# Optimization experiments

Hardware: AMD Instinct MI355X
Metric: run time of the kernel (lower is better)

Reference implementation:

```python
import jax, jax.numpy as jnp
import numpy as np

B, IH, IW = 16, 32, 32
N = IH * IW
HEADS, DIM_HEAD = 8, 64
INNER = HEADS * DIM_HEAD  # 512
INP, OUP = 512, 512
SCALE = DIM_HEAD ** -0.5


def _relative_index():
    # replicate torch.meshgrid (ij) -> coords [2, N]
    yy, xx = np.meshgrid(np.arange(IH), np.arange(IW), indexing='ij')
    coords = np.stack([yy.reshape(-1), xx.reshape(-1)])  # [2, N]
    rel = coords[:, :, None] - coords[:, None, :]        # [2, N, N]
    rel[0] += IH - 1
    rel[1] += IW - 1
    rel[0] *= 2 * IW - 1
    return jnp.asarray(rel.sum(0).reshape(-1), dtype=jnp.int32)  # [N*N]


def setup_inputs() -> dict:
    key = jax.random.key(0)
    k1, k2, k3, k4, k5 = jax.random.split(key, 5)
    x = jax.random.normal(k1, (B, N, INP), dtype=jnp.float32)
    W_qkv = jax.random.normal(k2, (INP, 3 * INNER), dtype=jnp.float32) * (INP ** -0.5)
    # table is initialized to zeros in the module; use small randn so bias path is exercised
    rel_table = jax.random.normal(k3, ((2 * IH - 1) * (2 * IW - 1), HEADS), dtype=jnp.float32) * 0.02
    W_out = jax.random.normal(k4, (INNER, OUP), dtype=jnp.float32) * (INNER ** -0.5)
    b_out = jax.random.normal(k5, (OUP,), dtype=jnp.float32) * 0.02
    return {
        'x': x,
        'W_qkv': W_qkv,
        'rel_table': rel_table,
        'W_out': W_out,
        'b_out': b_out,
        'rel_index': _relative_index(),
    }


def reference(x, W_qkv, rel_table, W_out, b_out, rel_index):
    b, n, _ = x.shape
    qkv = x @ W_qkv                                            # [b, n, 3*inner]
    q, k, v = jnp.split(qkv, 3, axis=-1)
    def to_heads(t):
        return t.reshape(b, n, HEADS, DIM_HEAD).transpose(0, 2, 1, 3)  # [b, h, n, d]
    q, k, v = to_heads(q), to_heads(k), to_heads(v)
    dots = jnp.einsum('bhnd,bhmd->bhnm', q, k) * SCALE         # [b, h, n, n]
    bias = rel_table[rel_index].reshape(n, n, HEADS).transpose(2, 0, 1)[None]  # [1, h, n, n]
    attn = jax.nn.softmax(dots + bias, axis=-1)
    out = jnp.einsum('bhnm,bhmd->bhnd', attn, v)               # [b, h, n, d]
    out = out.transpose(0, 2, 1, 3).reshape(b, n, INNER)       # [b, n, inner]
    return out @ W_out + b_out
```

## Files before the change

### kernel.cpp

```cpp
#include <hip/hip_runtime.h>
#include <math.h>

#define BATCH 16
#define NTOK 1024
#define HEADS 8
#define DHEAD 64
#define INNER 512
#define QKV_COLS 1536
#define SCALE_L2E 0.1803368801111244f
#define LOG2E 1.4426950408889634f

#if __has_builtin(__builtin_amdgcn_exp2f)
#define EXP2F(x) __builtin_amdgcn_exp2f(x)
#else
#define EXP2F(x) __expf((x) * 0.6931471805599453f)
#endif

typedef _Float16 f16x8 __attribute__((ext_vector_type(8)));
typedef _Float16 f16x4 __attribute__((ext_vector_type(4)));
typedef float f32x4 __attribute__((ext_vector_type(4)));

#define MFMA32(a, b, c) __builtin_amdgcn_mfma_f32_16x16x32_f16(a, b, c, 0, 0, 0)
#define MFMA16(a, b, c) __builtin_amdgcn_mfma_f32_16x16x16f16(a, b, c, 0, 0, 0)

__device__ __forceinline__ void glds16(const void* g, void* l) {
    __builtin_amdgcn_global_load_lds(
        (const __attribute__((address_space(1))) unsigned int*)g,
        (__attribute__((address_space(3))) unsigned int*)l, 16, 0, 0);
}

#define XV (BATCH * NTOK * INNER / 4)
#define WQ (INNER * QKV_COLS)
#define WO (INNER * INNER)

__global__ __launch_bounds__(256)
void convert_inputs(const float* __restrict__ x, const float* __restrict__ Wq,
                    const float* __restrict__ Wo, _Float16* __restrict__ x_h,
                    _Float16* __restrict__ Wq_t, _Float16* __restrict__ Wo_t) {
    int idx = blockIdx.x * 256 + threadIdx.x;
    if (idx < XV) {
        float4 v = ((const float4*)x)[idx];
        f16x4 h;
        h[0] = (_Float16)v.x; h[1] = (_Float16)v.y;
        h[2] = (_Float16)v.z; h[3] = (_Float16)v.w;
        *(f16x4*)(x_h + (size_t)idx * 4) = h;
    } else if (idx < XV + WQ) {
        int i = idx - XV;
        int n = i >> 9, k = i & 511;
        Wq_t[i] = (_Float16)Wq[k * QKV_COLS + n];
    } else if (idx < XV + WQ + WO) {
        int i = idx - XV - WQ;
        int n = i >> 9, k = i & 511;
        Wo_t[i] = (_Float16)Wo[k * INNER + n];
    }
}

template<bool OUT_F16, bool ADD_BIAS>
__global__ __launch_bounds__(256)
void gemm_f16(const _Float16* __restrict__ A, const _Float16* __restrict__ Bt,
              const float* __restrict__ bias, void* __restrict__ Cout,
              int M, int N, int K) {
    __shared__ _Float16 As[128 * 32];
    __shared__ _Float16 Bs[128 * 32];

    const int t    = threadIdx.x;
    const int l    = t & 63;
    const int w    = t >> 6;
    const int wm   = w >> 1;
    const int wn   = w & 1;
    const int quad = l >> 4;
    const int lrow = l & 15;
    const size_t row0 = (size_t)blockIdx.y * 128;
    const size_t col0 = (size_t)blockIdx.x * 128;

    const int srow = t >> 2;
    const int sch  = t & 3;

    f32x4 acc[4][4] = {};

    for (int k0 = 0; k0 < K; k0 += 32) {
        __syncthreads();
        glds16(A + (row0 + srow) * K + k0 + sch * 8,            (char*)As + t * 16);
        glds16(A + (row0 + 64 + srow) * K + k0 + sch * 8,       (char*)As + 4096 + t * 16);
        glds16(Bt + (col0 + srow) * K + k0 + sch * 8,           (char*)Bs + t * 16);
        glds16(Bt + (col0 + 64 + srow) * K + k0 + sch * 8,      (char*)Bs + 4096 + t * 16);
        __syncthreads();

        f16x8 af[4], bf[4];
#pragma unroll
        for (int i = 0; i < 4; ++i)
            af[i] = *(const f16x8*)(As + (wm * 64 + i * 16 + lrow) * 32 + quad * 8);
#pragma unroll
        for (int j = 0; j < 4; ++j)
            bf[j] = *(const f16x8*)(Bs + (wn * 64 + j * 16 + lrow) * 32 + quad * 8);
#pragma unroll
        for (int i = 0; i < 4; ++i)
#pragma unroll
            for (int j = 0; j < 4; ++j)
                acc[i][j] = __builtin_amdgcn_mfma_f32_16x16x32_f16(af[i], bf[j], acc[i][j], 0, 0, 0);
    }

#pragma unroll
    for (int i = 0; i < 4; ++i) {
#pragma unroll
        for (int j = 0; j < 4; ++j) {
            size_t r = row0 + wm * 64 + i * 16 + quad * 4;
            size_t c = col0 + wn * 64 + j * 16 + lrow;
#pragma unroll
            for (int reg = 0; reg < 4; ++reg) {
                float v = acc[i][j][reg];
                if (OUT_F16) {
                    ((_Float16*)Cout)[(r + reg) * N + c] = (_Float16)v;
                } else {
                    if (ADD_BIAS) v += bias[c];
                    ((float*)Cout)[(r + reg) * N + c] = v;
                }
            }
        }
    }
}

__global__ __launch_bounds__(256)
void transpose_v(const _Float16* __restrict__ qkv, _Float16* __restrict__ vt) {
    __shared__ _Float16 T[64][72];
    const int t  = threadIdx.x;
    const int j0 = blockIdx.x * 64;
    const int h  = blockIdx.y, bb = blockIdx.z;
    const int jr = t >> 2;
    const int dc = (t & 3) * 16;
    const _Float16* src = qkv + ((size_t)bb * NTOK + j0 + jr) * QKV_COLS + 2 * INNER + h * DHEAD + dc;
    f16x8 v0 = *(const f16x8*)src;
    f16x8 v1 = *(const f16x8*)(src + 8);
#pragma unroll
    for (int e = 0; e < 8; ++e) { T[jr][dc + e] = v0[e]; T[jr][dc + 8 + e] = v1[e]; }
    __syncthreads();
    const int dr = t >> 2;
    const int jc = (t & 3) * 16;
    f16x8 o0, o1;
#pragma unroll
    for (int e = 0; e < 8; ++e) { o0[e] = T[jc + e][dr]; o1[e] = T[jc + 8 + e][dr]; }
    _Float16* dst = vt + (((size_t)bb * HEADS + h) * 64 + dr) * NTOK + j0 + jc;
    *(f16x8*)dst = o0;
    *(f16x8*)(dst + 8) = o1;
}

__global__ __launch_bounds__(256, 4)
void attn_f16_v5(const _Float16* __restrict__ qkv, const _Float16* __restrict__ vt,
                 const float* __restrict__ rel_table, _Float16* __restrict__ out) {
    __shared__ _Float16 Ks[2][64 * 64];
    __shared__ _Float16 Vs[2][64 * 64];
    __shared__ _Float16 biasH[3969];

    const int t    = threadIdx.x;
    const int l    = t & 63;
    const int w    = t >> 6;
    const int quad = l >> 4;
    const int lrow = l & 15;
    const int h    = blockIdx.y;
    const int bb   = blockIdx.z;
    const int qr0  = blockIdx.x * 128 + w * 32;

    for (int idx = t; idx < 3969; idx += 256)
        biasH[idx] = (_Float16)(rel_table[idx * HEADS + h] * LOG2E);

    const size_t tokbase = (size_t)bb * NTOK;

    f16x8 aq[2][2];
#pragma unroll
    for (int mt = 0; mt < 2; ++mt)
#pragma unroll
        for (int ksi = 0; ksi < 2; ++ksi)
            aq[mt][ksi] = *(const f16x8*)(qkv + (tokbase + qr0 + mt * 16 + lrow) * QKV_COLS
                                          + h * DHEAD + ksi * 32 + quad * 8);

    f32x4 O[2][4] = {};
    float l0 = 0.f, l1 = 0.f;

    const int bconst = ((qr0 >> 5) + 31) * 63 + 31 + lrow - quad * 4;

    const int kr  = t >> 3;
    const int ksl = t & 7;
    const _Float16* kbase = qkv + tokbase * QKV_COLS + INNER + h * DHEAD;
    const _Float16* vbase = vt + ((size_t)(bb * HEADS + h) * 64) * NTOK;

    auto stage = [&](int jt, int bufi) {
        const int j0s = jt * 64;
        const int swz = (ksl ^ (kr & 7)) * 8;
        glds16(kbase + (size_t)(j0s + kr) * QKV_COLS + swz,      (char*)Ks[bufi] + t * 16);
        glds16(kbase + (size_t)(j0s + 32 + kr) * QKV_COLS + swz, (char*)Ks[bufi] + 4096 + t * 16);
        glds16(vbase + (size_t)kr * NTOK + j0s + swz,            (char*)Vs[bufi] + t * 16);
        glds16(vbase + (size_t)(32 + kr) * NTOK + j0s + swz,     (char*)Vs[bufi] + 4096 + t * 16);
    };

    stage(0, 0);

    for (int jt = 0; jt < 16; ++jt) {
        const int buf = jt & 1;
        __syncthreads();
        if (jt < 15) stage(jt + 1, buf ^ 1);

#pragma unroll
        for (int jn = 0; jn < 4; ++jn) {
            const int row = jn * 16 + lrow;
            f32x4 S0 = {}, S1 = {};
#pragma unroll
            for (int ksi = 0; ksi < 2; ++ksi) {
                f16x8 bk = *(const f16x8*)(Ks[buf] + row * 64 + (((ksi * 4 + quad) ^ (row & 7)) * 8));
                S0 = MFMA32(bk, aq[0][ksi], S0);
                S1 = MFMA32(bk, aq[1][ksi], S1);
            }

            const int base0 = bconst - (jt * 2 + (jn >> 1)) * 63 - (jn & 1) * 16;
            f16x4 pb0, pb1;
            {
                float p0 = EXP2F(fmaf(S0[0], SCALE_L2E, (float)biasH[base0 - 0]));
                float p1 = EXP2F(fmaf(S0[1], SCALE_L2E, (float)biasH[base0 - 1]));
                float p2 = EXP2F(fmaf(S0[2], SCALE_L2E, (float)biasH[base0 - 2]));
                float p3 = EXP2F(fmaf(S0[3], SCALE_L2E, (float)biasH[base0 - 3]));
                l0 += (p0 + p1) + (p2 + p3);
                pb0[0] = (_Float16)p0; pb0[1] = (_Float16)p1;
                pb0[2] = (_Float16)p2; pb0[3] = (_Float16)p3;
            }
            {
                const int base1 = base0 + 16;
                float p0 = EXP2F(fmaf(S1[0], SCALE_L2E, (float)biasH[base1 - 0]));
                float p1 = EXP2F(fmaf(S1[1], SCALE_L2E, (float)biasH[base1 - 1]));
                float p2 = EXP2F(fmaf(S1[2], SCALE_L2E, (float)biasH[base1 - 2]));
                float p3 = EXP2F(fmaf(S1[3], SCALE_L2E, (float)biasH[base1 - 3]));
                l1 += (p0 + p1) + (p2 + p3);
                pb1[0] = (_Float16)p0; pb1[1] = (_Float16)p1;
                pb1[2] = (_Float16)p2; pb1[3] = (_Float16)p3;
            }

#pragma unroll
            for (int dn = 0; dn < 4; ++dn) {
                const int d = dn * 16 + lrow;
                f16x4 av = *(const f16x4*)(Vs[buf] + d * 64
                              + (((jn * 2 + (quad >> 1)) ^ (d & 7)) * 8) + (quad & 1) * 4);
                O[0][dn] = MFMA16(av, pb0, O[0][dn]);
                O[1][dn] = MFMA16(av, pb1, O[1][dn]);
            }
        }
    }

#pragma unroll
    for (int mt = 0; mt < 2; ++mt) {
        float s = mt ? l1 : l0;
        s += __shfl_xor(s, 16);
        s += __shfl_xor(s, 32);
        const float inv = 1.f / s;
        const size_t orow = (tokbase + qr0 + mt * 16 + lrow) * INNER + h * DHEAD;
#pragma unroll
        for (int dn = 0; dn < 4; ++dn) {
            const f32x4 o = O[mt][dn];
            f16x4 ov;
            ov[0] = (_Float16)(o[0] * inv); ov[1] = (_Float16)(o[1] * inv);
            ov[2] = (_Float16)(o[2] * inv); ov[3] = (_Float16)(o[3] * inv);
            *(f16x4*)(out + orow + dn * 16 + quad * 4) = ov;
        }
    }
}

extern "C" void kernel_launch(void* const* d_in, const int* in_sizes, int n_in,
                              void* d_out, int out_size, void* d_ws, size_t ws_size,
                              hipStream_t stream) {
    const float* x         = (const float*)d_in[0];
    const float* W_qkv     = (const float*)d_in[1];
    const float* rel_table = (const float*)d_in[2];
    const float* W_out     = (const float*)d_in[3];
    const float* b_out     = (const float*)d_in[4];

    _Float16* x_h   = (_Float16*)d_ws;
    _Float16* Wq_t  = x_h + (size_t)BATCH * NTOK * INNER;
    _Float16* Wo_t  = Wq_t + (size_t)INNER * QKV_COLS;
    _Float16* qkv_h = Wo_t + (size_t)INNER * INNER;
    _Float16* att_h = qkv_h + (size_t)BATCH * NTOK * QKV_COLS;
    _Float16* vt_g  = att_h + (size_t)BATCH * NTOK * INNER;

    const int M = BATCH * NTOK;

    convert_inputs<<<(XV + WQ + WO + 255) / 256, 256, 0, stream>>>(
        x, W_qkv, W_out, x_h, Wq_t, Wo_t);

    gemm_f16<true, false><<<dim3(QKV_COLS / 128, M / 128), 256, 0, stream>>>(
        x_h, Wq_t, nullptr, qkv_h, M, QKV_COLS, INNER);

    transpose_v<<<dim3(NTOK / 64, HEADS, BATCH), 256, 0, stream>>>(qkv_h, vt_g);

    attn_f16_v5<<<dim3(NTOK / 128, HEADS, BATCH), 256, 0, stream>>>(
        qkv_h, vt_g, rel_table, att_h);

    gemm_f16<false, true><<<dim3(INNER / 128, M / 128), 256, 0, stream>>>(
        att_h, Wo_t, b_out, d_out, M, INNER, INNER);
}
```

Baseline: 243.5 us.

## Use 16x16x32 MFMA for PV with permuted K rows and 512-thread blocks

```diff
diff --git a/kernel.cpp b/kernel.cpp
--- a/kernel.cpp
+++ b/kernel.cpp
@@ -21,7 +21,6 @@
 typedef float f32x4 __attribute__((ext_vector_type(4)));
 
 #define MFMA32(a, b, c) __builtin_amdgcn_mfma_f32_16x16x32_f16(a, b, c, 0, 0, 0)
-#define MFMA16(a, b, c) __builtin_amdgcn_mfma_f32_16x16x16f16(a, b, c, 0, 0, 0)
 
 __device__ __forceinline__ void glds16(const void* g, void* l) {
     __builtin_amdgcn_global_load_lds(
@@ -144,12 +143,12 @@
     *(f16x8*)(dst + 8) = o1;
 }
 
-__global__ __launch_bounds__(256, 4)
-void attn_f16_v5(const _Float16* __restrict__ qkv, const _Float16* __restrict__ vt,
+__global__ __launch_bounds__(512, 4)
+void attn_f16_v6(const _Float16* __restrict__ qkv, const _Float16* __restrict__ vt,
                  const float* __restrict__ rel_table, _Float16* __restrict__ out) {
     __shared__ _Float16 Ks[2][64 * 64];
     __shared__ _Float16 Vs[2][64 * 64];
-    __shared__ _Float16 biasH[3969];
+    __shared__ float biasS[3969];
 
     const int t    = threadIdx.x;
     const int l    = t & 63;
@@ -158,10 +157,10 @@
     const int lrow = l & 15;
     const int h    = blockIdx.y;
     const int bb   = blockIdx.z;
-    const int qr0  = blockIdx.x * 128 + w * 32;
-
-    for (int idx = t; idx < 3969; idx += 256)
-        biasH[idx] = (_Float16)(rel_table[idx * HEADS + h] * LOG2E);
+    const int qr0  = blockIdx.x * 256 + w * 32;
+
+    for (int idx = t; idx < 3969; idx += 512)
+        biasS[idx] = rel_table[idx * HEADS + h] * LOG2E;
 
     const size_t tokbase = (size_t)bb * NTOK;
 
@@ -176,20 +175,20 @@
     f32x4 O[2][4] = {};
     float l0 = 0.f, l1 = 0.f;
 
-    const int bconst = ((qr0 >> 5) + 31) * 63 + 31 + lrow - quad * 4;
+    const int iy = qr0 >> 5;
+    const int krow_base = 8 * (lrow >> 2) + (lrow & 3);
+    const int fKl = (lrow & 3) + 4 * ((lrow >> 2) & 1);
 
     const int kr  = t >> 3;
     const int ksl = t & 7;
+    const int fKr = (kr & 3) + 4 * ((kr >> 3) & 1);
     const _Float16* kbase = qkv + tokbase * QKV_COLS + INNER + h * DHEAD;
     const _Float16* vbase = vt + ((size_t)(bb * HEADS + h) * 64) * NTOK;
 
     auto stage = [&](int jt, int bufi) {
         const int j0s = jt * 64;
-        const int swz = (ksl ^ (kr & 7)) * 8;
-        glds16(kbase + (size_t)(j0s + kr) * QKV_COLS + swz,      (char*)Ks[bufi] + t * 16);
-        glds16(kbase + (size_t)(j0s + 32 + kr) * QKV_COLS + swz, (char*)Ks[bufi] + 4096 + t * 16);
-        glds16(vbase + (size_t)kr * NTOK + j0s + swz,            (char*)Vs[bufi] + t * 16);
-        glds16(vbase + (size_t)(32 + kr) * NTOK + j0s + swz,     (char*)Vs[bufi] + 4096 + t * 16);
+        glds16(kbase + (size_t)(j0s + kr) * QKV_COLS + (ksl ^ fKr) * 8, (char*)Ks[bufi] + t * 16);
+        glds16(vbase + (size_t)kr * NTOK + j0s + (ksl ^ (kr & 7)) * 8,  (char*)Vs[bufi] + t * 16);
     };
 
     stage(0, 0);
@@ -200,45 +199,49 @@
         if (jt < 15) stage(jt + 1, buf ^ 1);
 
 #pragma unroll
-        for (int jn = 0; jn < 4; ++jn) {
-            const int row = jn * 16 + lrow;
-            f32x4 S0 = {}, S1 = {};
-#pragma unroll
-            for (int ksi = 0; ksi < 2; ++ksi) {
-                f16x8 bk = *(const f16x8*)(Ks[buf] + row * 64 + (((ksi * 4 + quad) ^ (row & 7)) * 8));
-                S0 = MFMA32(bk, aq[0][ksi], S0);
-                S1 = MFMA32(bk, aq[1][ksi], S1);
-            }
-
-            const int base0 = bconst - (jt * 2 + (jn >> 1)) * 63 - (jn & 1) * 16;
-            f16x4 pb0, pb1;
-            {
-                float p0 = EXP2F(fmaf(S0[0], SCALE_L2E, (float)biasH[base0 - 0]));
-                float p1 = EXP2F(fmaf(S0[1], SCALE_L2E, (float)biasH[base0 - 1]));
-                float p2 = EXP2F(fmaf(S0[2], SCALE_L2E, (float)biasH[base0 - 2]));
-                float p3 = EXP2F(fmaf(S0[3], SCALE_L2E, (float)biasH[base0 - 3]));
-                l0 += (p0 + p1) + (p2 + p3);
-                pb0[0] = (_Float16)p0; pb0[1] = (_Float16)p1;
-                pb0[2] = (_Float16)p2; pb0[3] = (_Float16)p3;
-            }
-            {
-                const int base1 = base0 + 16;
-                float p0 = EXP2F(fmaf(S1[0], SCALE_L2E, (float)biasH[base1 - 0]));
-                float p1 = EXP2F(fmaf(S1[1], SCALE_L2E, (float)biasH[base1 - 1]));
-                float p2 = EXP2F(fmaf(S1[2], SCALE_L2E, (float)biasH[base1 - 2]));
-                float p3 = EXP2F(fmaf(S1[3], SCALE_L2E, (float)biasH[base1 - 3]));
-                l1 += (p0 + p1) + (p2 + p3);
-                pb1[0] = (_Float16)p0; pb1[1] = (_Float16)p1;
-                pb1[2] = (_Float16)p2; pb1[3] = (_Float16)p3;
+        for (int jn0 = 0; jn0 < 2; ++jn0) {
+            f16x8 pb0, pb1;
+#pragma unroll
+            for (int s = 0; s < 2; ++s) {
+                const int krow = jn0 * 32 + krow_base + 4 * s;
+                f32x4 S0 = {}, S1 = {};
+#pragma unroll
+                for (int ksi = 0; ksi < 2; ++ksi) {
+                    f16x8 bk = *(const f16x8*)(Ks[buf] + krow * 64
+                                               + (((ksi * 4 + quad) ^ fKl) * 8));
+                    S0 = MFMA32(bk, aq[0][ksi], S0);
+                    S1 = MFMA32(bk, aq[1][ksi], S1);
+                }
+                const int base = (iy - (jt * 2 + jn0) + 31) * 63 + 31 + lrow
+                                 - 8 * quad - 4 * s;
+                {
+                    float p0 = EXP2F(fmaf(S0[0], SCALE_L2E, biasS[base - 0]));
+                    float p1 = EXP2F(fmaf(S0[1], SCALE_L2E, biasS[base - 1]));
+                    float p2 = EXP2F(fmaf(S0[2], SCALE_L2E, biasS[base - 2]));
+                    float p3 = EXP2F(fmaf(S0[3], SCALE_L2E, biasS[base - 3]));
+                    l0 += (p0 + p1) + (p2 + p3);
+                    pb0[s * 4 + 0] = (_Float16)p0; pb0[s * 4 + 1] = (_Float16)p1;
+                    pb0[s * 4 + 2] = (_Float16)p2; pb0[s * 4 + 3] = (_Float16)p3;
+                }
+                {
+                    const int b1 = base + 16;
+                    float p0 = EXP2F(fmaf(S1[0], SCALE_L2E, biasS[b1 - 0]));
+                    float p1 = EXP2F(fmaf(S1[1], SCALE_L2E, biasS[b1 - 1]));
+                    float p2 = EXP2F(fmaf(S1[2], SCALE_L2E, biasS[b1 - 2]));
+                    float p3 = EXP2F(fmaf(S1[3], SCALE_L2E, biasS[b1 - 3]));
+                    l1 += (p0 + p1) + (p2 + p3);
+                    pb1[s * 4 + 0] = (_Float16)p0; pb1[s * 4 + 1] = (_Float16)p1;
+                    pb1[s * 4 + 2] = (_Float16)p2; pb1[s * 4 + 3] = (_Float16)p3;
+                }
             }
 
 #pragma unroll
             for (int dn = 0; dn < 4; ++dn) {
                 const int d = dn * 16 + lrow;
-                f16x4 av = *(const f16x4*)(Vs[buf] + d * 64
-                              + (((jn * 2 + (quad >> 1)) ^ (d & 7)) * 8) + (quad & 1) * 4);
-                O[0][dn] = MFMA16(av, pb0, O[0][dn]);
-                O[1][dn] = MFMA16(av, pb1, O[1][dn]);
+                f16x8 av = *(const f16x8*)(Vs[buf] + d * 64
+                              + (((jn0 * 4 + quad) ^ (d & 7)) * 8));
+                O[0][dn] = MFMA32(av, pb0, O[0][dn]);
+                O[1][dn] = MFMA32(av, pb1, O[1][dn]);
             }
         }
     }
@@ -287,7 +290,7 @@
 
     transpose_v<<<dim3(NTOK / 64, HEADS, BATCH), 256, 0, stream>>>(qkv_h, vt_g);
 
-    attn_f16_v5<<<dim3(NTOK / 128, HEADS, BATCH), 256, 0, stream>>>(
+    attn_f16_v6<<<dim3(NTOK / 256, HEADS, BATCH), 512, 0, stream>>>(
         qkv_h, vt_g, rel_table, att_h);
 
     gemm_f16<false, true><<<dim3(INNER / 128, M / 128), 256, 0, stream>>>(
```

New measurement: 214.2 us. 1.14x faster.
